# Kernel tuning notes

Measured on AMD Instinct MI355X. Metric: run time of the kernel, lower is better.

The kernel has to match this reference:

```python
import jax, jax.numpy as jnp
import numpy as np

T, B, D, N = 512, 64, 1024, 64

def setup_inputs() -> dict:
    key = jax.random.key(0)
    kx, kw = jax.random.split(key)
    x = jax.random.normal(kx, (T, B, D), dtype=jnp.float32)
    # xavier-uniform per n_state-row block of W_kvqm: bound = sqrt(6/(N+D))
    bound = float(np.sqrt(6.0 / (N + D)))
    W_kvqm = jax.random.uniform(kw, (4 * N, D), dtype=jnp.float32, minval=-bound, maxval=bound)
    return {
        "x": x,
        "S0": jnp.zeros((B, N, N), dtype=jnp.float32),
        "M0": jnp.zeros((B, N, N), dtype=jnp.float32),
        "W_kvqm": W_kvqm,
        "B_S": jnp.full((N, N), 2.0, dtype=jnp.float32),
        "B_M": jnp.full((N, N), 2.5, dtype=jnp.float32),
    }

def _normalize(v):
    return v / (jnp.linalg.norm(v, axis=-1, keepdims=True) + 1e-6)

def reference(x, S0, M0, W_kvqm, B_S, B_M):
    n = B_S.shape[0]
    proj = jnp.einsum('tbd,nd->tbn', x, W_kvqm)  # [T,B,4n]
    k_all, v_all, q_all, m_all = jnp.split(proj, 4, axis=-1)

    def step(carry, inp):
        S, M = carry
        k, v, q, m_vec = inp
        k_n = _normalize(k)   # [B,n]
        m_n = _normalize(m_vec)
        # S update, gated by M
        M_k = jnp.einsum('bij,bj->bi', M, k_n)
        G_S = jax.nn.sigmoid(M + M_k[:, :, None] * k_n[:, None, :] + B_S)
        s_delta = v - jnp.einsum('bij,bj->bi', S, k_n)
        S = G_S * S + s_delta[:, :, None] * k_n[:, None, :]
        # M update, gated by new S
        S_m = jnp.einsum('bij,bj->bi', S, m_n)
        G_M = jax.nn.sigmoid(S + S_m[:, :, None] * m_n[:, None, :] + B_M)
        m_delta = s_delta - jnp.einsum('bij,bj->bi', M, m_n)
        M = G_M * M + m_delta[:, :, None] * m_n[:, None, :]
        # self-gated readout
        Sq = jnp.einsum('bij,bj->bi', S, q)
        out = Sq * jax.nn.silu(Sq)
        return (S, M), out

    (S, M), output = jax.lax.scan(step, (S0, M0), (k_all, v_all, q_all, m_all))
    return output, S, M
```

## Files before the change

kernel.cpp:

```cpp
#include <hip/hip_runtime.h>
#include <math.h>

#define TT 512
#define BB 64
#define DD 1024
#define NN 64
#define PC 256

__device__ __forceinline__ float fast_sigmoid(float x) {
    float e = __builtin_amdgcn_exp2f(x * -1.442695041f);
    return __builtin_amdgcn_rcpf(1.0f + e);
}

template<int C>
__device__ __forceinline__ float dpp_mov(float x) {
    return __int_as_float(__builtin_amdgcn_update_dpp(
        0, __float_as_int(x), C, 0xF, 0xF, true));
}
template<int P>
__device__ __forceinline__ float swz(float x) {
    return __int_as_float(__builtin_amdgcn_ds_swizzle(__float_as_int(x), P));
}
__device__ __forceinline__ float red32(float x) {
    x += dpp_mov<0xB1>(x);
    x += dpp_mov<0x4E>(x);
    x += swz<0x101F>(x);
    x += swz<0x201F>(x);
    x += swz<0x401F>(x);
    return x;
}

__global__ __launch_bounds__(256, 2) void proj_gemm(
    const float* __restrict__ X,
    const float* __restrict__ W,
    float* __restrict__ P)
{
    __shared__ float Xs[2][16][68];
    __shared__ float Ws[2][16][260];

    const int t    = threadIdx.x;
    const int row0 = blockIdx.x * 64;
    const int m4   = (t & 15) * 4;
    const int n16  = (t >> 4) * 16;
    const int lr   = t >> 2;
    const int lk   = (t & 3) * 4;

    float2 acc[4][8];
#pragma unroll
    for (int m = 0; m < 4; ++m)
#pragma unroll
        for (int j = 0; j < 8; ++j) acc[m][j] = make_float2(0.f, 0.f);

    const float* Xp = X + (long)(row0 + lr) * DD + lk;
    const float* Wp = W + (long)lr * DD + lk;

    float4 xv  = *(const float4*)(Xp);
    float4 wv0 = *(const float4*)(Wp);
    float4 wv1 = *(const float4*)(Wp + 64 * DD);
    float4 wv2 = *(const float4*)(Wp + 128 * DD);
    float4 wv3 = *(const float4*)(Wp + 192 * DD);

    for (int kt = 0; kt < 64; ++kt) {
        const int cur = kt & 1;
        Xs[cur][lk+0][lr] = xv.x; Xs[cur][lk+1][lr] = xv.y;
        Xs[cur][lk+2][lr] = xv.z; Xs[cur][lk+3][lr] = xv.w;
        Ws[cur][lk+0][lr]       = wv0.x; Ws[cur][lk+1][lr]       = wv0.y;
        Ws[cur][lk+2][lr]       = wv0.z; Ws[cur][lk+3][lr]       = wv0.w;
        Ws[cur][lk+0][lr + 64]  = wv1.x; Ws[cur][lk+1][lr + 64]  = wv1.y;
        Ws[cur][lk+2][lr + 64]  = wv1.z; Ws[cur][lk+3][lr + 64]  = wv1.w;
        Ws[cur][lk+0][lr + 128] = wv2.x; Ws[cur][lk+1][lr + 128] = wv2.y;
        Ws[cur][lk+2][lr + 128] = wv2.z; Ws[cur][lk+3][lr + 128] = wv2.w;
        Ws[cur][lk+0][lr + 192] = wv3.x; Ws[cur][lk+1][lr + 192] = wv3.y;
        Ws[cur][lk+2][lr + 192] = wv3.z; Ws[cur][lk+3][lr + 192] = wv3.w;

        if (kt < 63) {
            const int k0 = (kt + 1) * 16;
            xv  = *(const float4*)(Xp + k0);
            wv0 = *(const float4*)(Wp + k0);
            wv1 = *(const float4*)(Wp + 64 * DD + k0);
            wv2 = *(const float4*)(Wp + 128 * DD + k0);
            wv3 = *(const float4*)(Wp + 192 * DD + k0);
        }
        __syncthreads();

#pragma unroll
        for (int k = 0; k < 16; ++k) {
            const float4 a4 = *(const float4*)&Xs[cur][k][m4];
            const float4 b0 = *(const float4*)&Ws[cur][k][n16];
            const float4 b1 = *(const float4*)&Ws[cur][k][n16 + 4];
            const float4 b2 = *(const float4*)&Ws[cur][k][n16 + 8];
            const float4 b3 = *(const float4*)&Ws[cur][k][n16 + 12];
            const float av[4]  = {a4.x, a4.y, a4.z, a4.w};
            const float bv[16] = {b0.x,b0.y,b0.z,b0.w, b1.x,b1.y,b1.z,b1.w,
                                  b2.x,b2.y,b2.z,b2.w, b3.x,b3.y,b3.z,b3.w};
#pragma unroll
            for (int m = 0; m < 4; ++m)
#pragma unroll
                for (int j = 0; j < 8; ++j) {
                    acc[m][j].x = fmaf(av[m], bv[2*j],     acc[m][j].x);
                    acc[m][j].y = fmaf(av[m], bv[2*j + 1], acc[m][j].y);
                }
        }
    }

    const int wid = t >> 6;
    if (wid == 0 || wid == 3) {
#pragma unroll
        for (int m = 0; m < 4; ++m) {
            float p = 0.f;
#pragma unroll
            for (int j = 0; j < 8; ++j)
                p += acc[m][j].x * acc[m][j].x + acc[m][j].y * acc[m][j].y;
            p += swz<0x401F>(p);
            p += __shfl_xor(p, 32);
            const float inv = __builtin_amdgcn_rcpf(sqrtf(p) + 1e-6f);
#pragma unroll
            for (int j = 0; j < 8; ++j) { acc[m][j].x *= inv; acc[m][j].y *= inv; }
        }
    }

#pragma unroll
    for (int m = 0; m < 4; ++m) {
        float* Cp = P + (long)(row0 + m4 + m) * PC + n16;
#pragma unroll
        for (int g = 0; g < 4; ++g) {
            float4 o = make_float4(acc[m][2*g].x, acc[m][2*g].y,
                                   acc[m][2*g+1].x, acc[m][2*g+1].y);
            *(float4*)(Cp + 4*g) = o;
        }
    }
}

__global__ __launch_bounds__(256) void gate_scan(
    const float* __restrict__ P,
    const float* __restrict__ S0,
    const float* __restrict__ M0,
    const float* __restrict__ B_S,
    const float* __restrict__ B_M,
    float* __restrict__ out)
{
    const int bid  = blockIdx.x;
    const int grp  = bid >> 3;
    const int b    = (bid & 7) * 8 + (grp >> 3);
    const int sub  = grp & 7;
    const int w    = threadIdx.x >> 6;
    const int lane = threadIdx.x & 63;
    const int half = lane >> 5;
    const int li   = lane & 31;
    const int j0   = li * 2;
    const int r    = sub * 8 + w * 2 + half;

    float2 S2, M2, BS2, BM2;
    S2  = *(const float2*)(S0  + (long)b * 4096 + r * 64 + j0);
    M2  = *(const float2*)(M0  + (long)b * 4096 + r * 64 + j0);
    BS2 = *(const float2*)(B_S + r * 64 + j0);
    BM2 = *(const float2*)(B_M + r * 64 + j0);

    const float* Pb = P + (long)b * PC;
    const long   st = (long)BB * PC;

    float2 kn = *(const float2*)(Pb + j0);
    float2 q2 = *(const float2*)(Pb + 128 + j0);
    float2 mn = *(const float2*)(Pb + 192 + j0);
    float  vv = Pb[64 + r];

    for (int t = 0; t < TT; ++t) {
        const long nb = (long)((t + 1 < TT) ? t + 1 : t) * st;
        const float2 knn = *(const float2*)(Pb + nb + j0);
        const float2 qn  = *(const float2*)(Pb + nb + 128 + j0);
        const float2 mnn = *(const float2*)(Pb + nb + 192 + j0);
        const float  vvn = Pb[nb + 64 + r];

        float sk = fmaf(S2.y, kn.y, S2.x * kn.x);
        float mk = fmaf(M2.y, kn.y, M2.x * kn.x);
        sk = red32(sk);
        mk = red32(mk);
        const float sd = vv - sk;

        {
            const float g0 = fast_sigmoid(fmaf(mk, kn.x, M2.x + BS2.x));
            const float g1 = fast_sigmoid(fmaf(mk, kn.y, M2.y + BS2.y));
            S2.x = fmaf(g0, S2.x, sd * kn.x);
            S2.y = fmaf(g1, S2.y, sd * kn.y);
        }

        float sm = fmaf(S2.y, mn.y, S2.x * mn.x);
        float mv = fmaf(M2.y, mn.y, M2.x * mn.x);
        sm = red32(sm);
        mv = red32(mv);
        const float md = sd - mv;

        {
            const float g0 = fast_sigmoid(fmaf(sm, mn.x, S2.x + BM2.x));
            const float g1 = fast_sigmoid(fmaf(sm, mn.y, S2.y + BM2.y));
            M2.x = fmaf(g0, M2.x, md * mn.x);
            M2.y = fmaf(g1, M2.y, md * mn.y);
        }

        float sq = fmaf(S2.y, q2.y, S2.x * q2.x);
        sq = red32(sq);
        if (li == 0)
            out[((long)t * BB + b) * NN + r] = sq * sq * fast_sigmoid(sq);

        kn = knn; q2 = qn; mn = mnn; vv = vvn;
    }

    float* So = out + (long)TT * BB * NN + (long)b * 4096 + r * 64 + j0;
    float* Mo = So + (long)BB * 4096;
    *(float2*)So = S2;
    *(float2*)Mo = M2;
}

extern "C" void kernel_launch(void* const* d_in, const int* in_sizes, int n_in,
                              void* d_out, int out_size, void* d_ws, size_t ws_size,
                              hipStream_t stream) {
    const float* x    = (const float*)d_in[0];
    const float* S0   = (const float*)d_in[1];
    const float* M0   = (const float*)d_in[2];
    const float* W    = (const float*)d_in[3];
    const float* B_S  = (const float*)d_in[4];
    const float* B_M  = (const float*)d_in[5];
    float* out  = (float*)d_out;
    float* proj = (float*)d_ws;

    proj_gemm<<<512, 256, 0, stream>>>(x, W, proj);
    gate_scan<<<512, 256, 0, stream>>>(proj, S0, M0, B_S, B_M, out);
}
```

Measured before the change: 596.8 us.

## Retile projection GEMM to 128x128 blocks, use DPP reductions, reorder scan dot products

The projection GEMM switches from 64x256 tiles to 128x128 tiles with 8x8 register blocking, permuted shared-memory layout and a hand-written barrier. The k/m normalization now reduces partial row norms through shared memory. The scan replaces two ds_swizzle steps in the 32-lane reduction with DPP row shifts. It also hoists the M·m and S·q reductions so independent reductions interleave and the serial dependency chain per timestep gets shorter. This adds some per-step work and a more complex GEMM epilogue.

```diff
diff --git a/kernel.cpp b/kernel.cpp
--- a/kernel.cpp
+++ b/kernel.cpp
@@ -24,8 +24,8 @@
 __device__ __forceinline__ float red32(float x) {
     x += dpp_mov<0xB1>(x);
     x += dpp_mov<0x4E>(x);
-    x += swz<0x101F>(x);
-    x += swz<0x201F>(x);
+    x += dpp_mov<0x140>(x);
+    x += dpp_mov<0x128>(x);
     x += swz<0x401F>(x);
     return x;
 }
@@ -35,99 +35,116 @@
     const float* __restrict__ W,
     float* __restrict__ P)
 {
-    __shared__ float Xs[2][16][68];
-    __shared__ float Ws[2][16][260];
-
-    const int t    = threadIdx.x;
-    const int row0 = blockIdx.x * 64;
-    const int m4   = (t & 15) * 4;
-    const int n16  = (t >> 4) * 16;
-    const int lr   = t >> 2;
-    const int lk   = (t & 3) * 4;
-
-    float2 acc[4][8];
-#pragma unroll
-    for (int m = 0; m < 4; ++m)
-#pragma unroll
-        for (int j = 0; j < 8; ++j) acc[m][j] = make_float2(0.f, 0.f);
-
-    const float* Xp = X + (long)(row0 + lr) * DD + lk;
-    const float* Wp = W + (long)lr * DD + lk;
-
-    float4 xv  = *(const float4*)(Xp);
-    float4 wv0 = *(const float4*)(Wp);
-    float4 wv1 = *(const float4*)(Wp + 64 * DD);
-    float4 wv2 = *(const float4*)(Wp + 128 * DD);
-    float4 wv3 = *(const float4*)(Wp + 192 * DD);
+    __shared__ float Xs[2][16][132];
+    __shared__ float Ws[2][16][132];
+
+    const int t      = threadIdx.x;
+    const int rowblk = blockIdx.x >> 1;
+    const int colblk = blockIdx.x & 1;
+    const int row0   = rowblk * 128;
+    const int col0   = colblk * 128;
+    const int rg     = t & 15;
+    const int cg     = t >> 4;
+    const int m8     = rg * 8;
+    const int n8     = cg * 8;
+
+    const int lrow0 = t >> 2;
+    const int lrow1 = lrow0 + 64;
+    const int lkg   = (t & 3) * 4;
+
+    const float* Xp0 = X + (long)(row0 + lrow0) * DD + lkg;
+    const float* Xp1 = X + (long)(row0 + lrow1) * DD + lkg;
+    const float* Wp0 = W + (long)(col0 + lrow0) * DD + lkg;
+    const float* Wp1 = W + (long)(col0 + lrow1) * DD + lkg;
+
+    const int pc0 = ((lrow0 & 4) << 4) + ((lrow0 >> 3) << 2) + (lrow0 & 3);
+    const int pc1 = ((lrow1 & 4) << 4) + ((lrow1 >> 3) << 2) + (lrow1 & 3);
+
+    float acc[8][8];
+#pragma unroll
+    for (int u = 0; u < 8; ++u)
+#pragma unroll
+        for (int v = 0; v < 8; ++v) acc[u][v] = 0.f;
+
+    float4 x0 = *(const float4*)(Xp0);
+    float4 x1 = *(const float4*)(Xp1);
+    float4 w0 = *(const float4*)(Wp0);
+    float4 w1 = *(const float4*)(Wp1);
 
     for (int kt = 0; kt < 64; ++kt) {
         const int cur = kt & 1;
-        Xs[cur][lk+0][lr] = xv.x; Xs[cur][lk+1][lr] = xv.y;
-        Xs[cur][lk+2][lr] = xv.z; Xs[cur][lk+3][lr] = xv.w;
-        Ws[cur][lk+0][lr]       = wv0.x; Ws[cur][lk+1][lr]       = wv0.y;
-        Ws[cur][lk+2][lr]       = wv0.z; Ws[cur][lk+3][lr]       = wv0.w;
-        Ws[cur][lk+0][lr + 64]  = wv1.x; Ws[cur][lk+1][lr + 64]  = wv1.y;
-        Ws[cur][lk+2][lr + 64]  = wv1.z; Ws[cur][lk+3][lr + 64]  = wv1.w;
-        Ws[cur][lk+0][lr + 128] = wv2.x; Ws[cur][lk+1][lr + 128] = wv2.y;
-        Ws[cur][lk+2][lr + 128] = wv2.z; Ws[cur][lk+3][lr + 128] = wv2.w;
-        Ws[cur][lk+0][lr + 192] = wv3.x; Ws[cur][lk+1][lr + 192] = wv3.y;
-        Ws[cur][lk+2][lr + 192] = wv3.z; Ws[cur][lk+3][lr + 192] = wv3.w;
-
+        {
+            const float xa0[4] = {x0.x, x0.y, x0.z, x0.w};
+            const float xa1[4] = {x1.x, x1.y, x1.z, x1.w};
+            const float wa0[4] = {w0.x, w0.y, w0.z, w0.w};
+            const float wa1[4] = {w1.x, w1.y, w1.z, w1.w};
+#pragma unroll
+            for (int f = 0; f < 4; ++f) {
+                Xs[cur][lkg + f][pc0]   = xa0[f];
+                Xs[cur][lkg + f][pc1]   = xa1[f];
+                Ws[cur][lkg + f][lrow0] = wa0[f];
+                Ws[cur][lkg + f][lrow1] = wa1[f];
+            }
+        }
         if (kt < 63) {
             const int k0 = (kt + 1) * 16;
-            xv  = *(const float4*)(Xp + k0);
-            wv0 = *(const float4*)(Wp + k0);
-            wv1 = *(const float4*)(Wp + 64 * DD + k0);
-            wv2 = *(const float4*)(Wp + 128 * DD + k0);
-            wv3 = *(const float4*)(Wp + 192 * DD + k0);
-        }
-        __syncthreads();
+            x0 = *(const float4*)(Xp0 + k0);
+            x1 = *(const float4*)(Xp1 + k0);
+            w0 = *(const float4*)(Wp0 + k0);
+            w1 = *(const float4*)(Wp1 + k0);
+        }
+        asm volatile("s_waitcnt lgkmcnt(0)" ::: "memory");
+        __builtin_amdgcn_s_barrier();
+        asm volatile("" ::: "memory");
 
 #pragma unroll
         for (int k = 0; k < 16; ++k) {
-            const float4 a4 = *(const float4*)&Xs[cur][k][m4];
-            const float4 b0 = *(const float4*)&Ws[cur][k][n16];
-            const float4 b1 = *(const float4*)&Ws[cur][k][n16 + 4];
-            const float4 b2 = *(const float4*)&Ws[cur][k][n16 + 8];
-            const float4 b3 = *(const float4*)&Ws[cur][k][n16 + 12];
-            const float av[4]  = {a4.x, a4.y, a4.z, a4.w};
-            const float bv[16] = {b0.x,b0.y,b0.z,b0.w, b1.x,b1.y,b1.z,b1.w,
-                                  b2.x,b2.y,b2.z,b2.w, b3.x,b3.y,b3.z,b3.w};
-#pragma unroll
-            for (int m = 0; m < 4; ++m)
-#pragma unroll
-                for (int j = 0; j < 8; ++j) {
-                    acc[m][j].x = fmaf(av[m], bv[2*j],     acc[m][j].x);
-                    acc[m][j].y = fmaf(av[m], bv[2*j + 1], acc[m][j].y);
-                }
-        }
-    }
-
-    const int wid = t >> 6;
-    if (wid == 0 || wid == 3) {
-#pragma unroll
-        for (int m = 0; m < 4; ++m) {
+            const float4 alo = *(const float4*)&Xs[cur][k][rg * 4];
+            const float4 ahi = *(const float4*)&Xs[cur][k][64 + rg * 4];
+            const float4 blo = *(const float4*)&Ws[cur][k][n8];
+            const float4 bhi = *(const float4*)&Ws[cur][k][n8 + 4];
+            const float a[8] = {alo.x, alo.y, alo.z, alo.w,
+                                ahi.x, ahi.y, ahi.z, ahi.w};
+            const float b[8] = {blo.x, blo.y, blo.z, blo.w,
+                                bhi.x, bhi.y, bhi.z, bhi.w};
+#pragma unroll
+            for (int u = 0; u < 8; ++u)
+#pragma unroll
+                for (int v = 0; v < 8; ++v)
+                    acc[u][v] = fmaf(a[u], b[v], acc[u][v]);
+        }
+    }
+
+    __syncthreads();
+    float* scr = &Xs[0][0][0];
+    const bool sect = (colblk == 0) ? (cg < 8) : (cg >= 8);
+    if (sect) {
+#pragma unroll
+        for (int u = 0; u < 8; ++u) {
             float p = 0.f;
 #pragma unroll
-            for (int j = 0; j < 8; ++j)
-                p += acc[m][j].x * acc[m][j].x + acc[m][j].y * acc[m][j].y;
-            p += swz<0x401F>(p);
-            p += __shfl_xor(p, 32);
-            const float inv = __builtin_amdgcn_rcpf(sqrtf(p) + 1e-6f);
-#pragma unroll
-            for (int j = 0; j < 8; ++j) { acc[m][j].x *= inv; acc[m][j].y *= inv; }
-        }
-    }
-
-#pragma unroll
-    for (int m = 0; m < 4; ++m) {
-        float* Cp = P + (long)(row0 + m4 + m) * PC + n16;
-#pragma unroll
-        for (int g = 0; g < 4; ++g) {
-            float4 o = make_float4(acc[m][2*g].x, acc[m][2*g].y,
-                                   acc[m][2*g+1].x, acc[m][2*g+1].y);
-            *(float4*)(Cp + 4*g) = o;
-        }
+            for (int v = 0; v < 8; ++v) p += acc[u][v] * acc[u][v];
+            scr[(m8 + u) * 8 + (cg & 7)] = p;
+        }
+    }
+    __syncthreads();
+    if (sect) {
+#pragma unroll
+        for (int u = 0; u < 8; ++u) {
+            float s = 0.f;
+#pragma unroll
+            for (int j = 0; j < 8; ++j) s += scr[(m8 + u) * 8 + j];
+            const float inv = __builtin_amdgcn_rcpf(sqrtf(s) + 1e-6f);
+#pragma unroll
+            for (int v = 0; v < 8; ++v) acc[u][v] *= inv;
+        }
+    }
+
+#pragma unroll
+    for (int u = 0; u < 8; ++u) {
+        float* Cp = P + (long)(row0 + m8 + u) * PC + col0 + n8;
+        *(float4*)(Cp)     = make_float4(acc[u][0], acc[u][1], acc[u][2], acc[u][3]);
+        *(float4*)(Cp + 4) = make_float4(acc[u][4], acc[u][5], acc[u][6], acc[u][7]);
     }
 }
 
@@ -173,8 +190,10 @@
 
         float sk = fmaf(S2.y, kn.y, S2.x * kn.x);
         float mk = fmaf(M2.y, kn.y, M2.x * kn.x);
+        float mv = fmaf(M2.y, mn.y, M2.x * mn.x);
         sk = red32(sk);
         mk = red32(mk);
+        mv = red32(mv);
         const float sd = vv - sk;
 
         {
@@ -185,9 +204,9 @@
         }
 
         float sm = fmaf(S2.y, mn.y, S2.x * mn.x);
-        float mv = fmaf(M2.y, mn.y, M2.x * mn.x);
+        float sq = fmaf(S2.y, q2.y, S2.x * q2.x);
         sm = red32(sm);
-        mv = red32(mv);
+        sq = red32(sq);
         const float md = sd - mv;
 
         {
@@ -197,8 +216,6 @@
             M2.y = fmaf(g1, M2.y, md * mn.y);
         }
 
-        float sq = fmaf(S2.y, q2.y, S2.x * q2.x);
-        sq = red32(sq);
         if (li == 0)
             out[((long)t * BB + b) * NN + r] = sq * sq * fast_sigmoid(sq);
 
```

Result: faster. 568.6 us (-4.7%).
